# Kernel optimization log

Hardware: AMD Instinct MI355X
Metric: run time of the kernel (lower is better)

Reference implementation:

```python
import jax, jax.numpy as jnp
from jax import lax
import numpy as np

LATENT = 16
HIDDEN = 16  # latent_dim > 8 -> 16
NUM_ATTRACTORS = 64
GRAVITY = 0.01
INPUT_DIM = 300
B, S = 32, 2048
N_ITERS = 20


def setup_inputs() -> dict:
    key = jax.random.key(0)
    ks = jax.random.split(key, 12)
    sc = lambda fan_in: 1.0 / np.sqrt(fan_in)
    return {
        "inputs": jax.random.normal(ks[0], (B, S, INPUT_DIM), dtype=jnp.float32),
        "enc_w1": jax.random.normal(ks[1], (INPUT_DIM, HIDDEN), dtype=jnp.float32) * sc(INPUT_DIM),
        "enc_b1": jnp.zeros((HIDDEN,), dtype=jnp.float32),
        "enc_w2": jax.random.normal(ks[2], (HIDDEN, LATENT), dtype=jnp.float32) * sc(HIDDEN),
        "enc_b2": jnp.zeros((LATENT,), dtype=jnp.float32),
        "attractors": jax.random.normal(ks[3], (NUM_ATTRACTORS, LATENT), dtype=jnp.float32) * 0.1,
        "dec_w1": jax.random.normal(ks[4], (LATENT, HIDDEN), dtype=jnp.float32) * sc(LATENT),
        "dec_b1": jnp.zeros((HIDDEN,), dtype=jnp.float32),
        "dec_w2": jax.random.normal(ks[5], (HIDDEN, INPUT_DIM), dtype=jnp.float32) * sc(HIDDEN),
        "dec_b2": jnp.zeros((INPUT_DIM,), dtype=jnp.float32),
        "mass_w": jax.random.normal(ks[6], (LATENT, 1), dtype=jnp.float32) * sc(LATENT),
        "mass_b": jnp.zeros((1,), dtype=jnp.float32),
    }


def reference(inputs, enc_w1, enc_b1, enc_w2, enc_b2, attractors,
              dec_w1, dec_b1, dec_w2, dec_b2, mass_w, mass_b):
    b, s, _ = inputs.shape
    # encoder: Linear(300,16) -> ReLU -> Linear(16,latent)
    h = jax.nn.relu(jnp.einsum('bsi,ih->bsh', inputs, enc_w1) + enc_b1)
    emb = jnp.einsum('bsh,hd->bsd', h, enc_w2) + enc_b2  # [B,S,D]

    def step(pos, _):
        # pos: [B,S,D]; attractors: [A,D]
        diff = attractors[None, None, :, :] - pos[:, :, None, :]          # [B,S,A,D]
        dist = jnp.sqrt(jnp.sum(diff * diff, axis=-1, keepdims=True)) + 1e-6
        forces = jnp.sum(GRAVITY * diff / (dist * dist), axis=2)          # [B,S,D]
        new_pos = pos + 0.1 * forces
        change = jnp.sqrt(jnp.sum((new_pos - pos) ** 2))
        return new_pos, change

    # torch code breaks if change < 1e-6; with random data this never fires,
    # so the fixed 20-iteration scan is equivalent.
    positions, changes = lax.scan(step, emb, None, length=N_ITERS)

    attractor_field = positions.mean(axis=1)                              # [B,D]
    rec = jax.nn.relu(attractor_field @ dec_w1 + dec_b1) @ dec_w2 + dec_b2  # [B,300]
    reconstructions = jnp.broadcast_to(rec[:, None, :], (b, s, INPUT_DIM))
    masses = jax.nn.sigmoid(attractor_field @ mass_w + mass_b)            # [B,1]
    final_change = changes[-1]
    return attractor_field, reconstructions, masses, final_change
```

## Files before the change

### kernel.cpp

```cpp
#include <hip/hip_runtime.h>
#include <cmath>

#define BB 32
#define SS 2048
#define IND 300
#define HID 16
#define LAT 16
#define NA 64
#define NITER 20
#define GRAV 0.01f

#define OFF_FIELD 0
#define OFF_REC   512
#define OFF_MASS  (512 + BB*SS*IND)
#define OFF_CHG   (OFF_MASS + BB)

#define WS_FIELD 0
#define WS_CHG   512

typedef __attribute__((ext_vector_type(8))) __bf16 bf16x8;
typedef __attribute__((ext_vector_type(4))) __bf16 bf16x4;
typedef __attribute__((ext_vector_type(4))) float f32x4;

#define XST 328
#define HST 40
#define WTS 88

__global__ __launch_bounds__(256, 1)
void k_enc(const float* __restrict__ x, const float* __restrict__ w1,
           const float* __restrict__ b1, const float* __restrict__ w2,
           const float* __restrict__ b2, float* __restrict__ pbuf)
{
    __shared__ __align__(16) char smem[64 * XST * 2 + 4 * 16 * HST * 2];
    __bf16* xs = (__bf16*)smem;
    __bf16* hl = (__bf16*)(smem + 64 * XST * 2);

    const int tid  = threadIdx.x;
    const int wave = tid >> 6, lane = tid & 63;
    const int quad = lane >> 4, col = lane & 15;
    const int tok0 = blockIdx.x * 64;

    {
        const f32x4* xg = (const f32x4*)(x + (size_t)tok0 * IND);
        #pragma unroll
        for (int i = 0; i < 19; ++i) {
            const int idx = i * 256 + tid;
            if (idx < 4800) {
                f32x4 v = xg[idx];
                const int row = idx / 75, c4 = idx - row * 75;
                bf16x4 b;
                #pragma unroll
                for (int e = 0; e < 4; ++e) b[e] = (__bf16)v[e];
                *(bf16x4*)(xs + row * XST + c4 * 4) = b;
            }
        }
        if (tid < 64) {
            #pragma unroll
            for (int c = 0; c < 20; ++c) xs[tid * XST + 300 + c] = (__bf16)0.f;
        }
    }

    bf16x8 w1f[10];
    #pragma unroll
    for (int s = 0; s < 10; ++s)
        #pragma unroll
        for (int j = 0; j < 8; ++j) {
            const int k = s * 32 + quad * 8 + j;
            w1f[s][j] = (k < IND) ? (__bf16)w1[k * HID + col] : (__bf16)0.f;
        }
    __syncthreads();

    {
        const float b1c = b1[col];
        f32x4 hacc = {b1c, b1c, b1c, b1c};
        const __bf16* myx = xs + (wave * 16 + col) * XST + quad * 8;
        #pragma unroll
        for (int s = 0; s < 10; ++s) {
            bf16x8 af = *(const bf16x8*)(myx + s * 32);
            hacc = __builtin_amdgcn_mfma_f32_16x16x32_bf16(af, w1f[s], hacc, 0, 0, 0);
        }
        __bf16* myh = hl + wave * 16 * HST;
        #pragma unroll
        for (int r = 0; r < 4; ++r)
            myh[(quad * 4 + r) * HST + col] = (__bf16)fmaxf(hacc[r], 0.f);
    }

    f32x4 p;
    {
        bf16x8 w2tf;
        #pragma unroll
        for (int j = 0; j < 8; ++j) {
            const int k = quad * 8 + j;
            w2tf[j] = (k < HID) ? (__bf16)w2[k * LAT + col] : (__bf16)0.f;
        }
        bf16x8 bh;
        #pragma unroll
        for (int e = 0; e < 8; ++e) bh[e] = (__bf16)0.f;
        if (quad < 2)
            bh = *(const bf16x8*)(hl + wave * 16 * HST + col * HST + quad * 8);
        f32x4 pacc = *(const f32x4*)(b2 + quad * 4);
        p = __builtin_amdgcn_mfma_f32_16x16x32_bf16(w2tf, bh, pacc, 0, 0, 0);
    }
    ((f32x4*)pbuf)[(size_t)(tok0 + wave * 16 + col) * 4 + quad] = p;
}

__global__ __launch_bounds__(256, 1)
void k_grav(const float* __restrict__ att, const float* __restrict__ pbuf,
            float* __restrict__ ws)
{
    __shared__ __bf16 Wl[4][2][16 * WTS];
    const int tid  = threadIdx.x;
    const int wave = tid >> 6, lane = tid & 63;
    const int quad = lane >> 4, col = lane & 15;

    const f32x4 zf = {0.f, 0.f, 0.f, 0.f};
    bf16x8 ones8;
    #pragma unroll
    for (int e = 0; e < 8; ++e) ones8[e] = (__bf16)1.0f;

    bf16x8 aS[4];
    #pragma unroll
    for (int i = 0; i < 4; ++i) {
        f32x4 av = *(const f32x4*)(att + (16 * i + col) * LAT + quad * 4);
        #pragma unroll
        for (int m = 0; m < 4; ++m) {
            aS[i][2 * m]     = (__bf16)(-2.0f * av[m]);
            aS[i][2 * m + 1] = (__bf16)1.0f;
        }
    }
    f32x4 sanv[4];
    {
        float nrm[4];
        #pragma unroll
        for (int i = 0; i < 4; ++i) {
            const float* ar = att + (16 * i + col) * LAT;
            float s = 0.f;
            #pragma unroll
            for (int k = 0; k < LAT; ++k) s = fmaf(ar[k], ar[k], s);
            nrm[i] = s;
        }
        #pragma unroll
        for (int i = 0; i < 4; ++i)
            #pragma unroll
            for (int r = 0; r < 4; ++r)
                sanv[i][r] = __shfl(nrm[i], 16 * quad + quad * 4 + r);
    }
    bf16x8 aF[2];
    #pragma unroll
    for (int h = 0; h < 2; ++h)
        #pragma unroll
        for (int j = 0; j < 8; ++j)
            aF[h][j] = (__bf16)att[(32 * h + quad * 8 + j) * LAT + col];

    const int t0 = blockIdx.x * 128 + wave * 32 + col;
    f32x4 p[2];
    p[0] = ((const f32x4*)pbuf)[(size_t)t0 * 4 + quad];
    p[1] = ((const f32x4*)pbuf)[(size_t)(t0 + 16) * 4 + quad];

    __bf16* myW[2] = { &Wl[wave][0][0], &Wl[wave][1][0] };

    float cd = 0.f;
    #pragma unroll 1
    for (int it = 0; it < NITER; ++it) {
        bf16x8 bp[2];
        #pragma unroll
        for (int s = 0; s < 2; ++s)
            #pragma unroll
            for (int m = 0; m < 4; ++m) {
                float v = p[s][m];
                bp[s][2 * m]     = (__bf16)v;
                bp[s][2 * m + 1] = (__bf16)(v * v);
            }
        f32x4 sf[2][4];
        #pragma unroll
        for (int s = 0; s < 2; ++s)
            #pragma unroll
            for (int i = 0; i < 4; ++i)
                sf[s][i] = __builtin_amdgcn_mfma_f32_16x16x32_bf16(aS[i], bp[s], zf, 0, 0, 0);

        #pragma unroll
        for (int s = 0; s < 2; ++s)
            #pragma unroll
            for (int i = 0; i < 4; ++i) {
                bf16x4 wp;
                #pragma unroll
                for (int r = 0; r < 4; ++r)
                    wp[r] = (__bf16)__builtin_amdgcn_rcpf(sf[s][i][r] + sanv[i][r]);
                *(bf16x4*)(myW[s] + col * WTS + 16 * i + quad * 4) = wp;
            }
        bf16x8 bw[2][2];
        #pragma unroll
        for (int s = 0; s < 2; ++s)
            #pragma unroll
            for (int h = 0; h < 2; ++h)
                bw[s][h] = *(bf16x8*)(myW[s] + col * WTS + 32 * h + quad * 8);

        const bool last = (it == NITER - 1);
        #pragma unroll
        for (int s = 0; s < 2; ++s) {
            f32x4 F  = __builtin_amdgcn_mfma_f32_16x16x32_bf16(aF[0], bw[s][0], zf, 0, 0, 0);
            F  = __builtin_amdgcn_mfma_f32_16x16x32_bf16(aF[1], bw[s][1], F,  0, 0, 0);
            f32x4 F2 = __builtin_amdgcn_mfma_f32_16x16x32_bf16(ones8, bw[s][0], zf, 0, 0, 0);
            F2 = __builtin_amdgcn_mfma_f32_16x16x32_bf16(ones8, bw[s][1], F2, 0, 0, 0);
            #pragma unroll
            for (int r = 0; r < 4; ++r) {
                float np = fmaf(p[s][r], fmaf(F2[r], -0.1f * GRAV, 1.0f),
                                (0.1f * GRAV) * F[r]);
                if (last) { float d = np - p[s][r]; cd = fmaf(d, d, cd); }
                p[s][r] = np;
            }
        }
    }

    f32x4 fs;
    #pragma unroll
    for (int r = 0; r < 4; ++r) fs[r] = p[0][r] + p[1][r];
    #pragma unroll
    for (int m = 1; m <= 8; m <<= 1)
        #pragma unroll
        for (int r = 0; r < 4; ++r) fs[r] += __shfl_xor(fs[r], m);
    const int b = blockIdx.x >> 4;
    if (col == 0) {
        #pragma unroll
        for (int r = 0; r < 4; ++r)
            atomicAdd(ws + WS_FIELD + b * LAT + quad * 4 + r, fs[r]);
    }
    float c2 = cd;
    c2 += __shfl_xor(c2, 1);  c2 += __shfl_xor(c2, 2);  c2 += __shfl_xor(c2, 4);
    c2 += __shfl_xor(c2, 8);  c2 += __shfl_xor(c2, 16); c2 += __shfl_xor(c2, 32);
    if (lane == 0) atomicAdd(ws + WS_CHG, c2);
}

#define CHUNK 8192
#define CPB   (SS * IND / CHUNK)
__global__ __launch_bounds__(256)
void k_bcast(const float* __restrict__ dw1, const float* __restrict__ db1,
             const float* __restrict__ dw2, const float* __restrict__ db2,
             const float* __restrict__ mw,  const float* __restrict__ mb,
             const float* __restrict__ ws, float* __restrict__ out)
{
    __shared__ float sf[LAT];
    __shared__ float sh[HID];
    __shared__ __align__(16) float srow[IND];
    const int blk = blockIdx.x;
    const int b = blk / CPB, c = blk % CPB;
    const int t = threadIdx.x;

    if (t < LAT) {
        float f = ws[WS_FIELD + b * LAT + t] * (1.f / SS);
        sf[t] = f;
        if (c == 0) out[OFF_FIELD + b * LAT + t] = f;
    }
    __syncthreads();
    if (t < HID) {
        float a = db1[t];
        #pragma unroll
        for (int d = 0; d < LAT; ++d) a = fmaf(sf[d], dw1[d * HID + t], a);
        sh[t] = fmaxf(a, 0.f);
    }
    if (c == 0 && t == 32) {
        float a = mb[0];
        #pragma unroll
        for (int d = 0; d < LAT; ++d) a = fmaf(sf[d], mw[d], a);
        out[OFF_MASS + b] = 1.f / (1.f + expf(-a));
    }
    if (blk == 0 && t == 33) out[OFF_CHG] = sqrtf(ws[WS_CHG]);
    __syncthreads();
    if (t < IND) {
        float a = db2[t];
        #pragma unroll
        for (int j = 0; j < HID; ++j) a = fmaf(sh[j], dw2[j * IND + t], a);
        srow[t] = a;
    }
    if (t < IND - 256) {
        const int tc = t + 256;
        float a2 = db2[tc];
        #pragma unroll
        for (int j = 0; j < HID; ++j) a2 = fmaf(sh[j], dw2[j * IND + tc], a2);
        srow[tc] = a2;
    }
    __syncthreads();
    f32x4* o = (f32x4*)(out + OFF_REC + (size_t)b * (SS * IND) + (size_t)c * CHUNK);
    #pragma unroll
    for (int i = 0; i < CHUNK / 4 / 256; ++i) {
        const int o4 = i * 256 + t;
        const int r  = (c * CHUNK + o4 * 4) % IND;
        f32x4 v = *(const f32x4*)(srow + r);
        __builtin_nontemporal_store(v, o + o4);
    }
}

extern "C" void kernel_launch(void* const* d_in, const int* in_sizes, int n_in,
                              void* d_out, int out_size, void* d_ws, size_t ws_size,
                              hipStream_t stream)
{
    const float* x   = (const float*)d_in[0];
    const float* ew1 = (const float*)d_in[1];
    const float* eb1 = (const float*)d_in[2];
    const float* ew2 = (const float*)d_in[3];
    const float* eb2 = (const float*)d_in[4];
    const float* att = (const float*)d_in[5];
    const float* dw1 = (const float*)d_in[6];
    const float* db1 = (const float*)d_in[7];
    const float* dw2 = (const float*)d_in[8];
    const float* db2 = (const float*)d_in[9];
    const float* mw  = (const float*)d_in[10];
    const float* mb  = (const float*)d_in[11];
    float* out = (float*)d_out;
    float* ws  = (float*)d_ws;
    float* pbuf = out + OFF_REC;

    (void)hipMemsetAsync(ws, 0, (WS_CHG + 1) * sizeof(float), stream);
    k_enc <<<BB * SS / 64, 256, 0, stream>>>(x, ew1, eb1, ew2, eb2, pbuf);
    k_grav<<<BB * SS / 128, 256, 0, stream>>>(att, pbuf, ws);
    k_bcast<<<BB * CPB, 256, 0, stream>>>(dw1, db1, dw2, db2, mw, mb, ws, out);
}
```

Baseline: 217.5 us.

## Fuse encoder and gravity iteration into one kernel with direct global loads

Merges the encoder and the gravity-iteration kernels into a single kernel. Each wave encodes 16 tokens and keeps the latent positions in registers instead of writing them to a global buffer and reading them back. The encoder now loads x straight from global memory into MFMA operands instead of staging it in LDS, and occupancy is raised to 4 blocks per CU with one token group per wave. Per-block partial sums are reduced in shared memory before the atomics. The trade-offs are less instruction-level parallelism per wave in the iteration loop (one group instead of two) and W1 fragments reloaded from global memory inside the encoder loop.

```diff
diff --git a/kernel.cpp b/kernel.cpp
--- a/kernel.cpp
+++ b/kernel.cpp
@@ -22,71 +22,71 @@
 typedef __attribute__((ext_vector_type(4))) __bf16 bf16x4;
 typedef __attribute__((ext_vector_type(4))) float f32x4;
 
-#define XST 328
 #define HST 40
 #define WTS 88
 
-__global__ __launch_bounds__(256, 1)
-void k_enc(const float* __restrict__ x, const float* __restrict__ w1,
-           const float* __restrict__ b1, const float* __restrict__ w2,
-           const float* __restrict__ b2, float* __restrict__ pbuf)
+__global__ __launch_bounds__(256, 4)
+void k_fused(const float* __restrict__ x,  const float* __restrict__ w1,
+             const float* __restrict__ b1, const float* __restrict__ w2,
+             const float* __restrict__ b2, const float* __restrict__ att,
+             float* __restrict__ ws)
 {
-    __shared__ __align__(16) char smem[64 * XST * 2 + 4 * 16 * HST * 2];
-    __bf16* xs = (__bf16*)smem;
-    __bf16* hl = (__bf16*)(smem + 64 * XST * 2);
+    __shared__ __align__(16) __bf16 Wl[4][16 * WTS];
+    __shared__ __align__(16) __bf16 hl[4][16 * HST];
+    __shared__ float red[4][LAT];
+    __shared__ float redc[4];
 
     const int tid  = threadIdx.x;
     const int wave = tid >> 6, lane = tid & 63;
     const int quad = lane >> 4, col = lane & 15;
-    const int tok0 = blockIdx.x * 64;
-
+    const int tok  = blockIdx.x * 64 + wave * 16 + col;
+
+    f32x4 p;
     {
-        const f32x4* xg = (const f32x4*)(x + (size_t)tok0 * IND);
-        #pragma unroll
-        for (int i = 0; i < 19; ++i) {
-            const int idx = i * 256 + tid;
-            if (idx < 4800) {
-                f32x4 v = xg[idx];
-                const int row = idx / 75, c4 = idx - row * 75;
-                bf16x4 b;
-                #pragma unroll
-                for (int e = 0; e < 4; ++e) b[e] = (__bf16)v[e];
-                *(bf16x4*)(xs + row * XST + c4 * 4) = b;
-            }
-        }
-        if (tid < 64) {
-            #pragma unroll
-            for (int c = 0; c < 20; ++c) xs[tid * XST + 300 + c] = (__bf16)0.f;
-        }
-    }
-
-    bf16x8 w1f[10];
-    #pragma unroll
-    for (int s = 0; s < 10; ++s)
-        #pragma unroll
-        for (int j = 0; j < 8; ++j) {
-            const int k = s * 32 + quad * 8 + j;
-            w1f[s][j] = (k < IND) ? (__bf16)w1[k * HID + col] : (__bf16)0.f;
-        }
-    __syncthreads();
-
-    {
+        const float* xr = x + (size_t)tok * IND;
         const float b1c = b1[col];
         f32x4 hacc = {b1c, b1c, b1c, b1c};
-        const __bf16* myx = xs + (wave * 16 + col) * XST + quad * 8;
-        #pragma unroll
-        for (int s = 0; s < 10; ++s) {
-            bf16x8 af = *(const bf16x8*)(myx + s * 32);
-            hacc = __builtin_amdgcn_mfma_f32_16x16x32_bf16(af, w1f[s], hacc, 0, 0, 0);
-        }
-        __bf16* myh = hl + wave * 16 * HST;
+
+        #pragma unroll
+        for (int s = 0; s < 9; ++s) {
+            const float* xp = xr + s * 32 + quad * 8;
+            f32x4 lo = *(const f32x4*)(xp);
+            f32x4 hi = *(const f32x4*)(xp + 4);
+            bf16x8 af, wf;
+            #pragma unroll
+            for (int e = 0; e < 4; ++e) { af[e] = (__bf16)lo[e]; af[4 + e] = (__bf16)hi[e]; }
+            #pragma unroll
+            for (int j = 0; j < 8; ++j)
+                wf[j] = (__bf16)w1[(s * 32 + quad * 8 + j) * HID + col];
+            hacc = __builtin_amdgcn_mfma_f32_16x16x32_bf16(af, wf, hacc, 0, 0, 0);
+        }
+        {
+            bf16x8 af, wf;
+            #pragma unroll
+            for (int e = 0; e < 8; ++e) af[e] = (__bf16)0.f;
+            if (quad == 0) {
+                f32x4 lo = *(const f32x4*)(xr + 288);
+                f32x4 hi = *(const f32x4*)(xr + 292);
+                #pragma unroll
+                for (int e = 0; e < 4; ++e) { af[e] = (__bf16)lo[e]; af[4 + e] = (__bf16)hi[e]; }
+            } else if (quad == 1) {
+                f32x4 lo = *(const f32x4*)(xr + 296);
+                #pragma unroll
+                for (int e = 0; e < 4; ++e) af[e] = (__bf16)lo[e];
+            }
+            #pragma unroll
+            for (int j = 0; j < 8; ++j) {
+                const int k = 288 + quad * 8 + j;
+                wf[j] = (k < IND) ? (__bf16)w1[k * HID + col] : (__bf16)0.f;
+            }
+            hacc = __builtin_amdgcn_mfma_f32_16x16x32_bf16(af, wf, hacc, 0, 0, 0);
+        }
+
+        __bf16* myh = hl[wave];
         #pragma unroll
         for (int r = 0; r < 4; ++r)
             myh[(quad * 4 + r) * HST + col] = (__bf16)fmaxf(hacc[r], 0.f);
-    }
-
-    f32x4 p;
-    {
+
         bf16x8 w2tf;
         #pragma unroll
         for (int j = 0; j < 8; ++j) {
@@ -97,21 +97,10 @@
         #pragma unroll
         for (int e = 0; e < 8; ++e) bh[e] = (__bf16)0.f;
         if (quad < 2)
-            bh = *(const bf16x8*)(hl + wave * 16 * HST + col * HST + quad * 8);
+            bh = *(const bf16x8*)(myh + col * HST + quad * 8);
         f32x4 pacc = *(const f32x4*)(b2 + quad * 4);
         p = __builtin_amdgcn_mfma_f32_16x16x32_bf16(w2tf, bh, pacc, 0, 0, 0);
     }
-    ((f32x4*)pbuf)[(size_t)(tok0 + wave * 16 + col) * 4 + quad] = p;
-}
-
-__global__ __launch_bounds__(256, 1)
-void k_grav(const float* __restrict__ att, const float* __restrict__ pbuf,
-            float* __restrict__ ws)
-{
-    __shared__ __bf16 Wl[4][2][16 * WTS];
-    const int tid  = threadIdx.x;
-    const int wave = tid >> 6, lane = tid & 63;
-    const int quad = lane >> 4, col = lane & 15;
 
     const f32x4 zf = {0.f, 0.f, 0.f, 0.f};
     bf16x8 ones8;
@@ -152,83 +141,71 @@
         for (int j = 0; j < 8; ++j)
             aF[h][j] = (__bf16)att[(32 * h + quad * 8 + j) * LAT + col];
 
-    const int t0 = blockIdx.x * 128 + wave * 32 + col;
-    f32x4 p[2];
-    p[0] = ((const f32x4*)pbuf)[(size_t)t0 * 4 + quad];
-    p[1] = ((const f32x4*)pbuf)[(size_t)(t0 + 16) * 4 + quad];
-
-    __bf16* myW[2] = { &Wl[wave][0][0], &Wl[wave][1][0] };
-
+    __bf16* myW = Wl[wave];
     float cd = 0.f;
+
     #pragma unroll 1
     for (int it = 0; it < NITER; ++it) {
-        bf16x8 bp[2];
-        #pragma unroll
-        for (int s = 0; s < 2; ++s)
-            #pragma unroll
-            for (int m = 0; m < 4; ++m) {
-                float v = p[s][m];
-                bp[s][2 * m]     = (__bf16)v;
-                bp[s][2 * m + 1] = (__bf16)(v * v);
-            }
-        f32x4 sf[2][4];
-        #pragma unroll
-        for (int s = 0; s < 2; ++s)
-            #pragma unroll
-            for (int i = 0; i < 4; ++i)
-                sf[s][i] = __builtin_amdgcn_mfma_f32_16x16x32_bf16(aS[i], bp[s], zf, 0, 0, 0);
-
-        #pragma unroll
-        for (int s = 0; s < 2; ++s)
-            #pragma unroll
-            for (int i = 0; i < 4; ++i) {
-                bf16x4 wp;
-                #pragma unroll
-                for (int r = 0; r < 4; ++r)
-                    wp[r] = (__bf16)__builtin_amdgcn_rcpf(sf[s][i][r] + sanv[i][r]);
-                *(bf16x4*)(myW[s] + col * WTS + 16 * i + quad * 4) = wp;
-            }
-        bf16x8 bw[2][2];
-        #pragma unroll
-        for (int s = 0; s < 2; ++s)
-            #pragma unroll
-            for (int h = 0; h < 2; ++h)
-                bw[s][h] = *(bf16x8*)(myW[s] + col * WTS + 32 * h + quad * 8);
+        bf16x8 bp;
+        #pragma unroll
+        for (int m = 0; m < 4; ++m) {
+            float v = p[m];
+            bp[2 * m]     = (__bf16)v;
+            bp[2 * m + 1] = (__bf16)(v * v);
+        }
+        f32x4 sf[4];
+        #pragma unroll
+        for (int i = 0; i < 4; ++i)
+            sf[i] = __builtin_amdgcn_mfma_f32_16x16x32_bf16(aS[i], bp, zf, 0, 0, 0);
+
+        #pragma unroll
+        for (int i = 0; i < 4; ++i) {
+            bf16x4 wp;
+            #pragma unroll
+            for (int r = 0; r < 4; ++r)
+                wp[r] = (__bf16)__builtin_amdgcn_rcpf(sf[i][r] + sanv[i][r]);
+            *(bf16x4*)(myW + col * WTS + 16 * i + quad * 4) = wp;
+        }
+        bf16x8 bw0 = *(const bf16x8*)(myW + col * WTS + quad * 8);
+        bf16x8 bw1 = *(const bf16x8*)(myW + col * WTS + 32 + quad * 8);
+
+        f32x4 F  = __builtin_amdgcn_mfma_f32_16x16x32_bf16(aF[0], bw0, zf, 0, 0, 0);
+        F  = __builtin_amdgcn_mfma_f32_16x16x32_bf16(aF[1], bw1, F,  0, 0, 0);
+        f32x4 F2 = __builtin_amdgcn_mfma_f32_16x16x32_bf16(ones8, bw0, zf, 0, 0, 0);
+        F2 = __builtin_amdgcn_mfma_f32_16x16x32_bf16(ones8, bw1, F2, 0, 0, 0);
 
         const bool last = (it == NITER - 1);
         #pragma unroll
-        for (int s = 0; s < 2; ++s) {
-            f32x4 F  = __builtin_amdgcn_mfma_f32_16x16x32_bf16(aF[0], bw[s][0], zf, 0, 0, 0);
-            F  = __builtin_amdgcn_mfma_f32_16x16x32_bf16(aF[1], bw[s][1], F,  0, 0, 0);
-            f32x4 F2 = __builtin_amdgcn_mfma_f32_16x16x32_bf16(ones8, bw[s][0], zf, 0, 0, 0);
-            F2 = __builtin_amdgcn_mfma_f32_16x16x32_bf16(ones8, bw[s][1], F2, 0, 0, 0);
-            #pragma unroll
-            for (int r = 0; r < 4; ++r) {
-                float np = fmaf(p[s][r], fmaf(F2[r], -0.1f * GRAV, 1.0f),
-                                (0.1f * GRAV) * F[r]);
-                if (last) { float d = np - p[s][r]; cd = fmaf(d, d, cd); }
-                p[s][r] = np;
-            }
-        }
-    }
-
-    f32x4 fs;
-    #pragma unroll
-    for (int r = 0; r < 4; ++r) fs[r] = p[0][r] + p[1][r];
+        for (int r = 0; r < 4; ++r) {
+            float np = fmaf(p[r], fmaf(F2[r], -0.1f * GRAV, 1.0f),
+                            (0.1f * GRAV) * F[r]);
+            if (last) { float d = np - p[r]; cd = fmaf(d, d, cd); }
+            p[r] = np;
+        }
+    }
+
+    f32x4 fs = p;
     #pragma unroll
     for (int m = 1; m <= 8; m <<= 1)
         #pragma unroll
         for (int r = 0; r < 4; ++r) fs[r] += __shfl_xor(fs[r], m);
-    const int b = blockIdx.x >> 4;
     if (col == 0) {
         #pragma unroll
-        for (int r = 0; r < 4; ++r)
-            atomicAdd(ws + WS_FIELD + b * LAT + quad * 4 + r, fs[r]);
+        for (int r = 0; r < 4; ++r) red[wave][quad * 4 + r] = fs[r];
     }
     float c2 = cd;
     c2 += __shfl_xor(c2, 1);  c2 += __shfl_xor(c2, 2);  c2 += __shfl_xor(c2, 4);
     c2 += __shfl_xor(c2, 8);  c2 += __shfl_xor(c2, 16); c2 += __shfl_xor(c2, 32);
-    if (lane == 0) atomicAdd(ws + WS_CHG, c2);
+    if (lane == 0) redc[wave] = c2;
+    __syncthreads();
+
+    const int b = blockIdx.x >> 5;
+    if (tid < LAT) {
+        float v = red[0][tid] + red[1][tid] + red[2][tid] + red[3][tid];
+        atomicAdd(ws + WS_FIELD + b * LAT + tid, v);
+    }
+    if (tid == 32)
+        atomicAdd(ws + WS_CHG, redc[0] + redc[1] + redc[2] + redc[3]);
 }
 
 #define CHUNK 8192
@@ -308,10 +285,8 @@
     const float* mb  = (const float*)d_in[11];
     float* out = (float*)d_out;
     float* ws  = (float*)d_ws;
-    float* pbuf = out + OFF_REC;
 
     (void)hipMemsetAsync(ws, 0, (WS_CHG + 1) * sizeof(float), stream);
-    k_enc <<<BB * SS / 64, 256, 0, stream>>>(x, ew1, eb1, ew2, eb2, pbuf);
-    k_grav<<<BB * SS / 128, 256, 0, stream>>>(att, pbuf, ws);
+    k_fused<<<BB * SS / 64, 256, 0, stream>>>(x, ew1, eb1, ew2, eb2, att, ws);
     k_bcast<<<BB * CPB, 256, 0, stream>>>(dw1, db1, dw2, db2, mw, mb, ws, out);
 }
```

After: 190.3 us. 1.14x faster.
